# Kernel optimization log

Hardware: AMD Instinct MI355X
Metric: run time of the kernel (lower is better)

## Reference

```python
import jax, jax.numpy as jnp
import numpy as np

N = 50000   # nodes
E = 800000  # edges
F = 64      # feature dim (irreps_in = 64x0e)
M = 9       # spherical-harmonic dim (0e+1o+2e)
D = 32      # edge_attr_dim
H = 64      # MLP hidden
AVG_DEG = E / N


def setup_inputs() -> dict:
    key = jax.random.key(0)
    ks = jax.random.split(key, 14)
    features = jax.random.normal(ks[0], (N, F), jnp.float32)
    edge_index = jax.random.randint(ks[1], (2, E), 0, N)
    edge_attr = jax.random.normal(ks[2], (E, D), jnp.float32)
    edge_sh = jax.random.normal(ks[3], (E, M), jnp.float32)
    c_noise = jax.random.normal(ks[4], (N,), jnp.float32)
    # edge-weight MLP: edge_attr -> per-edge weights over SH paths
    W1 = jax.random.normal(ks[5], (D, H), jnp.float32) / np.sqrt(D)
    b1 = jnp.zeros((H,), jnp.float32)
    W2 = jax.random.normal(ks[6], (H, M), jnp.float32) / np.sqrt(H)
    b2 = jnp.zeros((M,), jnp.float32)
    # tensor-product mixing weights: (feat, sh) -> out feat
    W_tp = jax.random.normal(ks[7], (F, M, F), jnp.float32) / np.sqrt(F * M)
    # noise-conditional scaling MLP: c_noise -> (gamma, beta)
    Wn1 = jax.random.normal(ks[8], (1, H), jnp.float32)
    bn1 = jnp.zeros((H,), jnp.float32)
    Wn2 = jax.random.normal(ks[9], (H, 2 * F), jnp.float32) / np.sqrt(H)
    bn2 = jnp.zeros((2 * F,), jnp.float32)
    return dict(features=features, edge_index=edge_index, edge_attr=edge_attr,
                edge_sh=edge_sh, c_noise=c_noise, W1=W1, b1=b1, W2=W2, b2=b2,
                W_tp=W_tp, Wn1=Wn1, bn1=bn1, Wn2=Wn2, bn2=bn2)


def reference(features, edge_index, edge_attr, edge_sh, c_noise,
              W1, b1, W2, b2, W_tp, Wn1, bn1, Wn2, bn2):
    src, dst = edge_index[0], edge_index[1]
    # per-edge path weights from edge attributes: [E, M]
    w = jax.nn.silu(edge_attr @ W1 + b1) @ W2 + b2
    # gather source node features: [E, F]
    h_src = features[src]
    # weighted tensor product with spherical harmonics, mixed to out feats: [E, F]
    msg = jnp.einsum('ef,em,fmg->eg', h_src, edge_sh * w, W_tp)
    # scatter-sum to destination nodes, degree-normalized
    agg = jax.ops.segment_sum(msg, dst, num_segments=N) / jnp.sqrt(jnp.float32(AVG_DEG))
    # noise-conditional FiLM scaling
    emb = jax.nn.silu(c_noise[:, None] @ Wn1 + bn1) @ Wn2 + bn2  # [N, 2F]
    gamma, beta = jnp.split(emb, 2, axis=-1)
    return agg * (1.0 + gamma) + beta
```

## Files before the change

### kernel.cpp

```cpp
#include <hip/hip_runtime.h>
#include <hip/hip_bf16.h>

#define NN 50000
#define NE 800000

typedef unsigned int u32;
typedef unsigned short u16;
typedef __attribute__((ext_vector_type(2))) _Float16 half2v;
typedef __attribute__((ext_vector_type(8))) _Float16 half8;
typedef __attribute__((ext_vector_type(4))) float f32x4;

__device__ __forceinline__ float silu_f(float x) {
    return x * (1.0f / (1.0f + __expf(-x)));
}
__device__ __forceinline__ u16 f2h_bits(float f) {
    union { _Float16 h; u16 u; } c; c.h = (_Float16)f; return c.u;
}
__device__ __forceinline__ _Float16 h_from_bits(u16 u) {
    union { u16 u; _Float16 h; } c; c.u = u; return c.h;
}
__device__ __forceinline__ float h2f(u16 u) {
    return (float)h_from_bits(u);
}

__global__ __launch_bounds__(256) void k_scan_a(const u32* __restrict__ cnt, u32* __restrict__ part) {
    __shared__ u32 sb[256];
    int t = threadIdx.x, i = blockIdx.x * 256 + t;
    u32 v = (i < NN) ? cnt[i] : 0u;
    sb[t] = v; __syncthreads();
    for (int off = 128; off > 0; off >>= 1) { if (t < off) sb[t] += sb[t + off]; __syncthreads(); }
    if (t == 0) part[blockIdx.x] = sb[0];
}

__global__ __launch_bounds__(256) void k_scan_b(u32* __restrict__ part, int nparts) {
    __shared__ u32 sb[256];
    int t = threadIdx.x;
    u32 v = (t < nparts) ? part[t] : 0u;
    sb[t] = v; __syncthreads();
    for (int off = 1; off < 256; off <<= 1) {
        u32 x = (t >= off) ? sb[t - off] : 0u; __syncthreads();
        sb[t] += x; __syncthreads();
    }
    if (t < nparts) part[t] = sb[t] - v;
}

__global__ __launch_bounds__(256) void k_scan_c(const u32* __restrict__ cnt, const u32* __restrict__ part,
                                                u32* __restrict__ row, u32* __restrict__ rowcur) {
    __shared__ u32 sb[256];
    int t = threadIdx.x, i = blockIdx.x * 256 + t;
    u32 v = (i < NN) ? cnt[i] : 0u;
    sb[t] = v; __syncthreads();
    for (int off = 1; off < 256; off <<= 1) {
        u32 x = (t >= off) ? sb[t - off] : 0u; __syncthreads();
        sb[t] += x; __syncthreads();
    }
    if (i < NN) {
        u32 ex = part[blockIdx.x] + sb[t] - v;
        row[i] = ex; rowcur[i] = ex;
    }
    if (i == 0) row[NN] = NE;
}

__global__ __launch_bounds__(256) void k_prep_hist(const int* __restrict__ ei,
                                                   const float* __restrict__ feat,
                                                   const float* __restrict__ Wtp,
                                                   const float* __restrict__ W1,
                                                   const float* __restrict__ W2,
                                                   u32* __restrict__ cnt,
                                                   u16* __restrict__ feat16,
                                                   u16* __restrict__ WtT,
                                                   u16* __restrict__ W1T,
                                                   u16* __restrict__ W2T) {
    int o = blockIdx.x * 256 + threadIdx.x;
    if (o < 800000) {
        atomicAdd(&cnt[ei[NE + o]], 1u);
    } else if (o < 1200000) {
        int i = o - 800000;
        const float* fp = feat + (size_t)i * 8;
        float4 v0 = *(const float4*)fp;
        float4 v1 = *(const float4*)(fp + 4);
        ushort4 o0{f2h_bits(v0.x), f2h_bits(v0.y), f2h_bits(v0.z), f2h_bits(v0.w)};
        ushort4 o1{f2h_bits(v1.x), f2h_bits(v1.y), f2h_bits(v1.z), f2h_bits(v1.w)};
        u16* op = feat16 + (size_t)i * 8;
        *(ushort4*)op = o0;
        *(ushort4*)(op + 4) = o1;
    } else {
        int q = o - 1200000;
        if (q < 36864) {
            int g = q / 576, k = q % 576;
            int m = k >> 6, f = k & 63;
            WtT[q] = f2h_bits(Wtp[f * 576 + m * 64 + g]);
        } else if (q < 38912) {
            int i = q - 36864;
            int n = i >> 5, k = i & 31;
            W1T[i] = f2h_bits(W1[k * 64 + n]);
        } else if (q < 39936) {
            int i = q - 38912;
            int n = i >> 6, k = i & 63;
            W2T[i] = (n < 9) ? f2h_bits(W2[k * 9 + n]) : (u16)0;
        }
    }
}

__global__ __launch_bounds__(256, 2) void k_edge_mlp(
    const float* __restrict__ edge_attr, const float* __restrict__ edge_sh,
    const int* __restrict__ ei,
    const u16* __restrict__ W1T, const u16* __restrict__ W2T,
    const float* __restrict__ b1, const float* __restrict__ b2,
    u32* __restrict__ rowcur, u32* __restrict__ ssd,
    u16* __restrict__ s_sorted)
{
    __shared__ u16 sW1[64 * 36];
    __shared__ u16 sW2[16 * 68];
    __shared__ u16 sHid[4][64 * 68];
    __shared__ u16 sWout[256 * 12];
    const int t  = threadIdx.x;
    const int w  = t >> 6;
    const int l  = t & 63;
    const int e0 = blockIdx.x * 256;
    const int wbase = w << 6;

    const int eIdx = e0 + t;
    const u32 s_ = (u32)ei[eIdx];
    const u32 d_ = (u32)ei[NE + eIdx];
    const u32 pos = atomicAdd(&rowcur[d_], 1u);
    ssd[pos] = s_ | (d_ << 16);

    {
        const u32* g1 = (const u32*)W1T;
        u32* l1 = (u32*)sW1;
        #pragma unroll
        for (int i = 0; i < 4; ++i) {
            int idx = i * 256 + t;
            int r = idx >> 4, c = idx & 15;
            l1[r * 18 + c] = g1[idx];
        }
        const u32* g2 = (const u32*)W2T;
        u32* l2 = (u32*)sW2;
        #pragma unroll
        for (int i = 0; i < 2; ++i) {
            int idx = i * 256 + t;
            int r = idx >> 5, c = idx & 31;
            l2[r * 34 + c] = g2[idx];
        }
    }

    half8 aA[4];
    #pragma unroll
    for (int et = 0; et < 4; ++et) {
        const int e = e0 + wbase + (et << 4) + (l & 15);
        const float* ap = edge_attr + (size_t)e * 32 + ((l >> 4) << 3);
        float4 v0 = *(const float4*)ap;
        float4 v1 = *(const float4*)(ap + 4);
        aA[et] = half8{(_Float16)v0.x, (_Float16)v0.y, (_Float16)v0.z, (_Float16)v0.w,
                       (_Float16)v1.x, (_Float16)v1.y, (_Float16)v1.z, (_Float16)v1.w};
    }
    __syncthreads();

    f32x4 acc1[4][4] = {};
    {
        half8 bB[4];
        #pragma unroll
        for (int nt = 0; nt < 4; ++nt)
            bB[nt] = *(const half8*)&sW1[((nt << 4) + (l & 15)) * 36 + ((l >> 4) << 3)];
        #pragma unroll
        for (int et = 0; et < 4; ++et)
            #pragma unroll
            for (int nt = 0; nt < 4; ++nt)
                acc1[et][nt] = __builtin_amdgcn_mfma_f32_16x16x32_f16(aA[et], bB[nt], acc1[et][nt], 0, 0, 0);
    }

    {
        float b1v[4];
        #pragma unroll
        for (int nt = 0; nt < 4; ++nt) b1v[nt] = b1[(nt << 4) + (l & 15)];
        #pragma unroll
        for (int et = 0; et < 4; ++et)
            #pragma unroll
            for (int nt = 0; nt < 4; ++nt)
                #pragma unroll
                for (int rg = 0; rg < 4; ++rg) {
                    int r = (et << 4) + ((l >> 4) << 2) + rg;
                    int c = (nt << 4) + (l & 15);
                    sHid[w][r * 68 + c] = f2h_bits(silu_f(acc1[et][nt][rg] + b1v[nt]));
                }
    }
    __syncthreads();

    f32x4 acc2[4] = {};
    #pragma unroll
    for (int tt = 0; tt < 2; ++tt) {
        half8 b2f = *(const half8*)&sW2[(l & 15) * 68 + tt * 32 + ((l >> 4) << 3)];
        #pragma unroll
        for (int et = 0; et < 4; ++et) {
            half8 a2 = *(const half8*)&sHid[w][((et << 4) + (l & 15)) * 68 + tt * 32 + ((l >> 4) << 3)];
            acc2[et] = __builtin_amdgcn_mfma_f32_16x16x32_f16(a2, b2f, acc2[et], 0, 0, 0);
        }
    }

    {
        const int m = l & 15;
        if (m < 9) {
            const float b2v = b2[m];
            #pragma unroll
            for (int et = 0; et < 4; ++et)
                #pragma unroll
                for (int rg = 0; rg < 4; ++rg) {
                    int r = wbase + (et << 4) + ((l >> 4) << 2) + rg;
                    sWout[r * 12 + m] = f2h_bits(acc2[et][rg] + b2v);
                }
        }
    }
    __syncthreads();

    const size_t e = (size_t)eIdx;
    const float* sh = edge_sh + e * 9;
    u16 sw[12];
    #pragma unroll
    for (int m = 0; m < 9; ++m) sw[m] = f2h_bits(sh[m] * h2f(sWout[t * 12 + m]));
    sw[9] = sw[10] = sw[11] = 0;

    u16* dp = s_sorted + (size_t)pos * 12;
    ushort4 v0{sw[0], sw[1], sw[2],  sw[3]};
    ushort4 v1{sw[4], sw[5], sw[6],  sw[7]};
    ushort4 v2{sw[8], sw[9], sw[10], sw[11]};
    *(ushort4*)(dp + 0) = v0;
    *(ushort4*)(dp + 4) = v1;
    *(ushort4*)(dp + 8) = v2;
}

union SmU {
    u16 wt[64 * 584];
    u16 msg[256 * 68];
};

__global__ __launch_bounds__(512, 2) void k_combine_mfma(
    const u32* __restrict__ ssd,  const u32* __restrict__ row,
    const u16* __restrict__ s_sorted,
    const u16* __restrict__ feat16, const u16* __restrict__ WtT,
    float* __restrict__ out)
{
    __shared__ SmU sm;
    const int t  = threadIdx.x;
    const int w  = t >> 6;
    const int l  = t & 63;
    const int p0 = blockIdx.x * 256;
    const int rbase = w << 5;

    u32 srcr[2];
    #pragma unroll
    for (int et = 0; et < 2; ++et)
        srcr[et] = ssd[p0 + rbase + (et << 4) + (l & 15)] & 0xFFFFu;

    half8 h16[2][2];
    #pragma unroll
    for (int et = 0; et < 2; ++et)
        #pragma unroll
        for (int fh = 0; fh < 2; ++fh)
            h16[et][fh] = *(const half8*)(feat16 +
                (size_t)srcr[et] * 64 + (fh << 5) + ((l >> 4) << 3));

    half2v s2[2][9];
    #pragma unroll
    for (int et = 0; et < 2; ++et) {
        const u16* sp = s_sorted + (size_t)(p0 + rbase + (et << 4) + (l & 15)) * 12;
        ushort4 sa = *(const ushort4*)(sp + 0);
        ushort4 sb = *(const ushort4*)(sp + 4);
        ushort4 sc = *(const ushort4*)(sp + 8);
        u16 sv[9] = {sa.x, sa.y, sa.z, sa.w, sb.x, sb.y, sb.z, sb.w, sc.x};
        #pragma unroll
        for (int m = 0; m < 9; ++m) {
            _Float16 h = h_from_bits(sv[m]);
            s2[et][m] = half2v{h, h};
        }
    }

    {
        const uint4* gsrc = (const uint4*)WtT;
        uint4* lw = (uint4*)sm.wt;
        #pragma unroll
        for (int i = 0; i < 9; ++i) {
            int c = i * 512 + t;
            int r = c / 72, q = c - r * 72;
            lw[r * 73 + q] = gsrc[c];
        }
    }
    __syncthreads();

    half8 bA[4], bB_[4];
    #pragma unroll
    for (int gt = 0; gt < 4; ++gt)
        bA[gt] = *(const half8*)&sm.wt[(((gt << 4) + (l & 15)) * 584) + ((l >> 4) << 3)];

    f32x4 acc[2][4] = {};
    #pragma unroll
    for (int j = 0; j < 18; ++j) {
        const int fh = (j < 9) ? 0 : 1;
        const int m  = (j < 9) ? j : j - 9;
        half8* cur = (j & 1) ? bB_ : bA;
        half8* nxt = (j & 1) ? bA  : bB_;
        if (j < 17) {
            const int jn  = j + 1;
            const int ttn = (jn < 9) ? (jn << 1) : (((jn - 9) << 1) + 1);
            #pragma unroll
            for (int gt = 0; gt < 4; ++gt)
                nxt[gt] = *(const half8*)&sm.wt[
                    (((gt << 4) + (l & 15)) * 584) + ttn * 32 + ((l >> 4) << 3)];
        }
        #pragma unroll
        for (int et = 0; et < 2; ++et) {
            union { half2v h2[4]; half8 v; } A;
            const union { half8 v; half2v h2[4]; } H = { h16[et][fh] };
            A.h2[0] = H.h2[0] * s2[et][m];
            A.h2[1] = H.h2[1] * s2[et][m];
            A.h2[2] = H.h2[2] * s2[et][m];
            A.h2[3] = H.h2[3] * s2[et][m];
            #pragma unroll
            for (int gt = 0; gt < 4; ++gt)
                acc[et][gt] = __builtin_amdgcn_mfma_f32_16x16x32_f16(A.v, cur[gt], acc[et][gt], 0, 0, 0);
        }
    }
    __syncthreads();

    #pragma unroll
    for (int et = 0; et < 2; ++et)
        #pragma unroll
        for (int gt = 0; gt < 4; ++gt)
            #pragma unroll
            for (int rg = 0; rg < 4; ++rg) {
                int rloc = rbase + (et << 4) + ((l >> 4) << 2) + rg;
                int col  = (gt << 4) + (l & 15);
                sm.msg[rloc * 68 + col] = f2h_bits(acc[et][gt][rg]);
            }
    __syncthreads();

    const int dfirst = (int)(ssd[p0] >> 16);
    const int dlast  = (int)(ssd[p0 + 255] >> 16);
    for (int n = dfirst + w; n <= dlast; n += 8) {
        int a = (int)row[n]     - p0; if (a < 0)   a = 0;
        int b = (int)row[n + 1] - p0; if (b > 256) b = 256;
        if (a < b) {
            float v = 0.f;
            for (int p = a; p < b; ++p) v += h2f(sm.msg[p * 68 + l]);
            atomicAdd(out + (size_t)n * 64 + l, v * 0.25f);
        }
    }
}

__global__ __launch_bounds__(256) void k_film(
    const float* __restrict__ c_noise,
    const float* __restrict__ Wn1, const float* __restrict__ bn1,
    const float* __restrict__ Wn2, const float* __restrict__ bn2,
    float* __restrict__ out)
{
    const int n    = (blockIdx.x * 256 + threadIdx.x) >> 6;
    const int lane = threadIdx.x & 63;
    const float c  = c_noise[n];
    const float hid = silu_f(fmaf(c, Wn1[lane], bn1[lane]));
    float g = bn2[lane], b = bn2[64 + lane];
    for (int h = 0; h < 64; ++h) {
        const float hv = __shfl(hid, h, 64);
        g = fmaf(hv, Wn2[h * 128 + lane],      g);
        b = fmaf(hv, Wn2[h * 128 + 64 + lane], b);
    }
    const size_t i = (size_t)n * 64 + lane;
    out[i] = fmaf(out[i], 1.f + g, b);
}

extern "C" void kernel_launch(void* const* d_in, const int* in_sizes, int n_in,
                              void* d_out, int out_size, void* d_ws, size_t ws_size,
                              hipStream_t stream) {
    const float* features   = (const float*)d_in[0];
    const int*   edge_index = (const int*)  d_in[1];
    const float* edge_attr  = (const float*)d_in[2];
    const float* edge_sh    = (const float*)d_in[3];
    const float* c_noise    = (const float*)d_in[4];
    const float* W1  = (const float*)d_in[5];
    const float* b1  = (const float*)d_in[6];
    const float* W2  = (const float*)d_in[7];
    const float* b2  = (const float*)d_in[8];
    const float* Wtp = (const float*)d_in[9];
    const float* Wn1 = (const float*)d_in[10];
    const float* bn1 = (const float*)d_in[11];
    const float* Wn2 = (const float*)d_in[12];
    const float* bn2 = (const float*)d_in[13];
    float* out = (float*)d_out;

    char* ws = (char*)d_ws;
    u16* feat16   = (u16*)(ws);
    u16* s_sorted = (u16*)(ws +  6400000);
    u32* ssd      = (u32*)(ws + 25600000);
    u32* row      = (u32*)(ws + 28800000);
    u32* rowcur   = (u32*)(ws + 29000016);
    u32* cnt      = (u32*)(ws + 29200016);
    u32* part     = (u32*)(ws + 29400016);
    u16* WtT      = (u16*)(ws + 29401040);
    u16* W1T      = (u16*)(ws + 29474768);
    u16* W2T      = (u16*)(ws + 29478864);

    const int nparts = (NN + 255) / 256;

    hipMemsetAsync(cnt, 0, (size_t)NN * 4, stream);
    hipMemsetAsync(out, 0, (size_t)NN * 64 * sizeof(float), stream);

    k_prep_hist<<<(1239936 + 255) / 256, 256, 0, stream>>>(
        edge_index, features, Wtp, W1, W2, cnt, feat16, WtT, W1T, W2T);

    k_scan_a <<<nparts, 256, 0, stream>>>(cnt, part);
    k_scan_b <<<1, 256, 0, stream>>>(part, nparts);
    k_scan_c <<<nparts, 256, 0, stream>>>(cnt, part, row, rowcur);

    k_edge_mlp<<<NE / 256, 256, 0, stream>>>(edge_attr, edge_sh, edge_index,
                                             W1T, W2T, b1, b2,
                                             rowcur, ssd, s_sorted);

    k_combine_mfma<<<NE / 256, 512, 0, stream>>>(ssd, row, s_sorted,
                                                 feat16, WtT, out);

    k_film<<<(NN * 64) / 256, 256, 0, stream>>>(c_noise, Wn1, bn1, Wn2, bn2, out);
}
```

Baseline: 252.9 us.

## Aggregate SH-weighted features per destination node before the W_tp MFMA

Result: slower. 441.6 us (+74.6%).

```diff
diff --git a/kernel.cpp b/kernel.cpp
--- a/kernel.cpp
+++ b/kernel.cpp
@@ -229,121 +229,84 @@
     *(ushort4*)(dp + 8) = v2;
 }
 
-union SmU {
-    u16 wt[64 * 584];
-    u16 msg[256 * 68];
-};
-
-__global__ __launch_bounds__(512, 2) void k_combine_mfma(
+__global__ __launch_bounds__(512, 2) void k_combine_q(
     const u32* __restrict__ ssd,  const u32* __restrict__ row,
     const u16* __restrict__ s_sorted,
     const u16* __restrict__ feat16, const u16* __restrict__ WtT,
     float* __restrict__ out)
 {
-    __shared__ SmU sm;
+    __shared__ u16 wt_s[64 * 584];
+    __shared__ u16 q_s[32 * 584];
     const int t  = threadIdx.x;
     const int w  = t >> 6;
     const int l  = t & 63;
     const int p0 = blockIdx.x * 256;
-    const int rbase = w << 5;
-
-    u32 srcr[2];
-    #pragma unroll
-    for (int et = 0; et < 2; ++et)
-        srcr[et] = ssd[p0 + rbase + (et << 4) + (l & 15)] & 0xFFFFu;
-
-    half8 h16[2][2];
-    #pragma unroll
-    for (int et = 0; et < 2; ++et)
-        #pragma unroll
-        for (int fh = 0; fh < 2; ++fh)
-            h16[et][fh] = *(const half8*)(feat16 +
-                (size_t)srcr[et] * 64 + (fh << 5) + ((l >> 4) << 3));
-
-    half2v s2[2][9];
-    #pragma unroll
-    for (int et = 0; et < 2; ++et) {
-        const u16* sp = s_sorted + (size_t)(p0 + rbase + (et << 4) + (l & 15)) * 12;
-        ushort4 sa = *(const ushort4*)(sp + 0);
-        ushort4 sb = *(const ushort4*)(sp + 4);
-        ushort4 sc = *(const ushort4*)(sp + 8);
-        u16 sv[9] = {sa.x, sa.y, sa.z, sa.w, sb.x, sb.y, sb.z, sb.w, sc.x};
-        #pragma unroll
-        for (int m = 0; m < 9; ++m) {
-            _Float16 h = h_from_bits(sv[m]);
-            s2[et][m] = half2v{h, h};
-        }
-    }
-
+
+    {
+        u32* qz = (u32*)q_s;
+        #pragma unroll
+        for (int i = 0; i < 19; ++i) {
+            int idx = i * 512 + t;
+            if (idx < 9344) qz[idx] = 0u;
+        }
+    }
     {
         const uint4* gsrc = (const uint4*)WtT;
-        uint4* lw = (uint4*)sm.wt;
+        uint4* lw = (uint4*)wt_s;
         #pragma unroll
         for (int i = 0; i < 9; ++i) {
             int c = i * 512 + t;
-            int r = c / 72, q = c - r * 72;
-            lw[r * 73 + q] = gsrc[c];
-        }
-    }
-    __syncthreads();
-
-    half8 bA[4], bB_[4];
-    #pragma unroll
-    for (int gt = 0; gt < 4; ++gt)
-        bA[gt] = *(const half8*)&sm.wt[(((gt << 4) + (l & 15)) * 584) + ((l >> 4) << 3)];
-
-    f32x4 acc[2][4] = {};
-    #pragma unroll
-    for (int j = 0; j < 18; ++j) {
-        const int fh = (j < 9) ? 0 : 1;
-        const int m  = (j < 9) ? j : j - 9;
-        half8* cur = (j & 1) ? bB_ : bA;
-        half8* nxt = (j & 1) ? bA  : bB_;
-        if (j < 17) {
-            const int jn  = j + 1;
-            const int ttn = (jn < 9) ? (jn << 1) : (((jn - 9) << 1) + 1);
-            #pragma unroll
-            for (int gt = 0; gt < 4; ++gt)
-                nxt[gt] = *(const half8*)&sm.wt[
-                    (((gt << 4) + (l & 15)) * 584) + ttn * 32 + ((l >> 4) << 3)];
-        }
-        #pragma unroll
-        for (int et = 0; et < 2; ++et) {
-            union { half2v h2[4]; half8 v; } A;
-            const union { half8 v; half2v h2[4]; } H = { h16[et][fh] };
-            A.h2[0] = H.h2[0] * s2[et][m];
-            A.h2[1] = H.h2[1] * s2[et][m];
-            A.h2[2] = H.h2[2] * s2[et][m];
-            A.h2[3] = H.h2[3] * s2[et][m];
-            #pragma unroll
-            for (int gt = 0; gt < 4; ++gt)
-                acc[et][gt] = __builtin_amdgcn_mfma_f32_16x16x32_f16(A.v, cur[gt], acc[et][gt], 0, 0, 0);
-        }
-    }
-    __syncthreads();
-
-    #pragma unroll
-    for (int et = 0; et < 2; ++et)
-        #pragma unroll
-        for (int gt = 0; gt < 4; ++gt)
-            #pragma unroll
-            for (int rg = 0; rg < 4; ++rg) {
-                int rloc = rbase + (et << 4) + ((l >> 4) << 2) + rg;
-                int col  = (gt << 4) + (l & 15);
-                sm.msg[rloc * 68 + col] = f2h_bits(acc[et][gt][rg]);
-            }
-    __syncthreads();
-
+            int rr = c / 72, qq = c - rr * 72;
+            lw[rr * 73 + qq] = gsrc[c];
+        }
+    }
     const int dfirst = (int)(ssd[p0] >> 16);
     const int dlast  = (int)(ssd[p0 + 255] >> 16);
+    __syncthreads();
+
     for (int n = dfirst + w; n <= dlast; n += 8) {
         int a = (int)row[n]     - p0; if (a < 0)   a = 0;
         int b = (int)row[n + 1] - p0; if (b > 256) b = 256;
-        if (a < b) {
-            float v = 0.f;
-            for (int p = a; p < b; ++p) v += h2f(sm.msg[p * 68 + l]);
-            atomicAdd(out + (size_t)n * 64 + l, v * 0.25f);
-        }
+        if (a >= b) continue;
+        const int r = n - dfirst;
+        if (r > 31) continue;
+        float q[9] = {0.f,0.f,0.f,0.f,0.f,0.f,0.f,0.f,0.f};
+        for (int p = a; p < b; ++p) {
+            const u32 sd = ssd[p0 + p];
+            const float hv = h2f(feat16[(size_t)(sd & 0xFFFFu) * 64 + l]);
+            const u16* sp = s_sorted + (size_t)(p0 + p) * 12;
+            ushort4 sa = *(const ushort4*)(sp);
+            ushort4 sb = *(const ushort4*)(sp + 4);
+            u16 s8 = sp[8];
+            q[0] = fmaf(h2f(sa.x), hv, q[0]);
+            q[1] = fmaf(h2f(sa.y), hv, q[1]);
+            q[2] = fmaf(h2f(sa.z), hv, q[2]);
+            q[3] = fmaf(h2f(sa.w), hv, q[3]);
+            q[4] = fmaf(h2f(sb.x), hv, q[4]);
+            q[5] = fmaf(h2f(sb.y), hv, q[5]);
+            q[6] = fmaf(h2f(sb.z), hv, q[6]);
+            q[7] = fmaf(h2f(sb.w), hv, q[7]);
+            q[8] = fmaf(h2f(s8),   hv, q[8]);
+        }
+        u16* qr = q_s + r * 584;
+        #pragma unroll
+        for (int m = 0; m < 9; ++m) qr[m * 64 + l] = f2h_bits(q[m]);
+    }
+    __syncthreads();
+
+    const int et = w >> 2, gt = w & 3;
+    f32x4 acc = {};
+    #pragma unroll
+    for (int tt = 0; tt < 18; ++tt) {
+        half8 a8 = *(const half8*)&q_s[((et << 4) + (l & 15)) * 584 + tt * 32 + ((l >> 4) << 3)];
+        half8 b8 = *(const half8*)&wt_s[((gt << 4) + (l & 15)) * 584 + tt * 32 + ((l >> 4) << 3)];
+        acc = __builtin_amdgcn_mfma_f32_16x16x32_f16(a8, b8, acc, 0, 0, 0);
+    }
+    #pragma unroll
+    for (int rg = 0; rg < 4; ++rg) {
+        const int n = dfirst + (et << 4) + ((l >> 4) << 2) + rg;
+        if (n <= dlast)
+            atomicAdd(out + (size_t)n * 64 + (gt << 4) + (l & 15), acc[rg] * 0.25f);
     }
 }
 
@@ -414,8 +377,8 @@
                                              W1T, W2T, b1, b2,
                                              rowcur, ssd, s_sorted);
 
-    k_combine_mfma<<<NE / 256, 512, 0, stream>>>(ssd, row, s_sorted,
-                                                 feat16, WtT, out);
+    k_combine_q<<<NE / 256, 512, 0, stream>>>(ssd, row, s_sorted,
+                                              feat16, WtT, out);
 
     k_film<<<(NN * 64) / 256, 256, 0, stream>>>(c_noise, Wn1, bn1, Wn2, bn2, out);
 }
```
